# Kernel tuning notes

Measured on AMD Instinct MI355X. Metric: run time of the kernel, lower is better.

Reference implementation:

```python
import jax, jax.numpy as jnp
import numpy as np

B, S, D, H = 64, 512, 544, 1024  # batch, seq, state_dim+pb_dim, n_hid


def setup_inputs() -> dict:
    key = jax.random.key(0)
    k_x, k_wih, k_whh, k_bih, k_bhh = jax.random.split(key, 5)
    bound = 1.0 / np.sqrt(H)  # PyTorch LSTM uniform init range
    X = jax.random.normal(k_x, (B, S, D), dtype=jnp.float32)
    W_ih = jax.random.uniform(k_wih, (4 * H, D), jnp.float32, -bound, bound)
    W_hh = jax.random.uniform(k_whh, (4 * H, H), jnp.float32, -bound, bound)
    b_ih = jax.random.uniform(k_bih, (4 * H,), jnp.float32, -bound, bound)
    b_hh = jax.random.uniform(k_bhh, (4 * H,), jnp.float32, -bound, bound)
    return {"X": X, "W_ih": W_ih, "W_hh": W_hh, "b_ih": b_ih, "b_hh": b_hh}


def reference(X, W_ih, W_hh, b_ih, b_hh):
    # Faithful to PBRNN.forward: LSTM scanned over the sequence dim
    # (the torch code loops one timestep at a time; the math is a plain
    # single-layer LSTM from zero initial state). Returns final (h, c)
    # stacked as [2, B, H] — the only state forward() produces.
    n_batch = X.shape[0]
    n_hid = W_hh.shape[1]
    Xs = jnp.swapaxes(X, 0, 1)  # [S, B, D]
    # Precompute input projections for all timesteps: [S, B, 4H]
    x_proj = jnp.einsum('sbd,gd->sbg', Xs, W_ih) + (b_ih + b_hh)

    def step(carry, xp):
        h, c = carry
        gates = xp + h @ W_hh.T  # [B, 4H]
        i, f, g, o = jnp.split(gates, 4, axis=-1)  # PyTorch gate order i,f,g,o
        i = jax.nn.sigmoid(i)
        f = jax.nn.sigmoid(f)
        g = jnp.tanh(g)
        o = jax.nn.sigmoid(o)
        c = f * c + i * g
        h = o * jnp.tanh(c)
        return (h, c), None

    h0 = jnp.zeros((n_batch, n_hid), dtype=X.dtype)
    c0 = jnp.zeros((n_batch, n_hid), dtype=X.dtype)
    (h_n, c_n), _ = jax.lax.scan(step, (h0, c0), x_proj)
    return jnp.stack([h_n, c_n])  # [2, B, H]
```

## Files before the change

kernel.cpp:

```cpp
#include <hip/hip_runtime.h>
#include <hip/hip_bf16.h>


#define B_  64
#define S_  512
#define D_  544
#define H_  1024
#define CG_ 64
#define BG_ 4
#define GRID_ (CG_*BG_)

typedef __attribute__((ext_vector_type(8))) short bf16x8;
typedef __attribute__((ext_vector_type(4))) float f32x4;

__device__ inline ushort f2b(float x){
  unsigned u = __float_as_uint(x);
  u = (u + 0x7FFFu + ((u >> 16) & 1u)) >> 16;
  return (ushort)u;
}

__device__ inline bf16x8 pack8(float4 a, float4 b){
  bf16x8 r;
  r[0]=(short)f2b(a.x); r[1]=(short)f2b(a.y); r[2]=(short)f2b(a.z); r[3]=(short)f2b(a.w);
  r[4]=(short)f2b(b.x); r[5]=(short)f2b(b.y); r[6]=(short)f2b(b.z); r[7]=(short)f2b(b.w);
  return r;
}

__device__ inline unsigned long long ld64a(const unsigned long long* q){
  return __hip_atomic_load(q, __ATOMIC_RELAXED, __HIP_MEMORY_SCOPE_AGENT);
}

__device__ inline float sigm(float x){ return __builtin_amdgcn_rcpf(1.f + __expf(-x)); }
__device__ inline float tanh_(float x){ return 1.f - 2.f*__builtin_amdgcn_rcpf(1.f + __expf(2.f*x)); }

__global__ void cvt_x(const float* __restrict__ x, ushort* __restrict__ xb, int n4){
  int i = blockIdx.x*256 + threadIdx.x;
  if (i >= n4) return;
  float4 v = ((const float4*)x)[i];
  ushort4 o;
  o.x=f2b(v.x); o.y=f2b(v.y); o.z=f2b(v.z); o.w=f2b(v.w);
  ((ushort4*)xb)[i] = o;
}

__global__ __launch_bounds__(256,1) void lstm_persist(
    const float* __restrict__ Wih, const float* __restrict__ Whh,
    const float* __restrict__ bih, const float* __restrict__ bhh,
    const ushort* __restrict__ Xb,
    unsigned* thbuf,
    float* __restrict__ out)
{
  const int tid  = threadIdx.x;
  const int wave = tid >> 6;
  const int lane = tid & 63;
  const int c16  = lane & 15;
  const int quad = lane >> 4;
  const int cg   = blockIdx.x & (CG_-1);
  const int bg   = blockIdx.x >> 6;

  __shared__ float gates_s[4][64][17];

  bf16x8 whhf[4][8];
  #pragma unroll
  for (int mt = 0; mt < 4; ++mt){
    const size_t grow = (size_t)(mt*H_ + cg*16 + c16);
    #pragma unroll
    for (int i = 0; i < 8; ++i){
      int k = wave*256 + i*32 + quad*8;
      const float4* p = (const float4*)(Whh + grow*H_ + k);
      whhf[mt][i] = pack8(p[0], p[1]);
    }
  }
  bf16x8 wihf[4][5];
  #pragma unroll
  for (int mt = 0; mt < 4; ++mt){
    const size_t grow = (size_t)(mt*H_ + cg*16 + c16);
    #pragma unroll
    for (int ii = 0; ii < 5; ++ii){
      int it = wave + 4*ii;
      if (it < 17){
        int k = it*32 + quad*8;
        const float4* p = (const float4*)(Wih + grow*D_ + k);
        wihf[mt][ii] = pack8(p[0], p[1]);
      }
    }
  }

  const int uu = tid & 15;
  const int nn = tid >> 4;
  float bsum[4];
  #pragma unroll
  for (int g = 0; g < 4; ++g)
    bsum[g] = bih[g*H_ + cg*16 + uu] + bhh[g*H_ + cg*16 + uu];
  float cstate = 0.f;

  f32x4 acc[4];

  auto zacc = [&]{
    #pragma unroll
    for (int mt = 0; mt < 4; ++mt) acc[mt] = (f32x4){0.f,0.f,0.f,0.f};
  };
  auto xp_gemm = [&](int t){
    #pragma unroll
    for (int ii = 0; ii < 5; ++ii){
      int it = wave + 4*ii;
      if (it < 17){
        int k = it*32 + quad*8;
        bf16x8 b = *(const bf16x8*)(Xb + ((size_t)(bg*16 + c16)*S_ + t)*D_ + k);
        #pragma unroll
        for (int mt = 0; mt < 4; ++mt)
          acc[mt] = __builtin_amdgcn_mfma_f32_16x16x32_bf16(wihf[mt][ii], b, acc[mt], 0,0,0);
      }
    }
  };

  zacc();
  xp_gemm(0);

  const int obase = (bg*64 + wave*16 + (quad>>1))*256 + c16*16 + (quad&1)*8;

  for (int t = 0; t < S_; ++t){
    const unsigned* hp = thbuf + (t & 1) * (B_*H_);
    unsigned*       hn = thbuf + ((t & 1) ^ 1) * (B_*H_);

    {
      const unsigned tag = (unsigned)t & 0xffffu;
      const unsigned long long tmask = 0xffff0000ffff0000ull;
      const unsigned long long texp  = ((unsigned long long)tag << 16)
                                     | ((unsigned long long)tag << 48);
      unsigned long long q[8][4];
      #pragma unroll
      for (int i = 0; i < 8; ++i){
        const unsigned long long* p = (const unsigned long long*)(hp + obase + i*512);
        q[i][0] = ld64a(p);   q[i][1] = ld64a(p+1);
        q[i][2] = ld64a(p+2); q[i][3] = ld64a(p+3);
      }
      #pragma unroll
      for (int i = 0; i < 8; ++i){
        const unsigned long long* p = (const unsigned long long*)(hp + obase + i*512);
        long guard = 0;
        while ((((q[i][0]^texp)|(q[i][1]^texp)|(q[i][2]^texp)|(q[i][3]^texp)) & tmask) != 0ull){
          q[i][0] = ld64a(p);   q[i][1] = ld64a(p+1);
          q[i][2] = ld64a(p+2); q[i][3] = ld64a(p+3);
          if (++guard > (1L<<20)) break;
        }
        union { unsigned u[4]; bf16x8 v8; } eb;
        #pragma unroll
        for (int w = 0; w < 4; ++w){
          unsigned lo = (unsigned)q[i][w];
          unsigned hi = (unsigned)(q[i][w] >> 32);
          eb.u[w] = (lo & 0xffffu) | (hi << 16);
        }
        #pragma unroll
        for (int mt = 0; mt < 4; ++mt)
          acc[mt] = __builtin_amdgcn_mfma_f32_16x16x32_bf16(whhf[mt][i], eb.v8, acc[mt], 0,0,0);
      }
    }

    #pragma unroll
    for (int mt = 0; mt < 4; ++mt)
      #pragma unroll
      for (int r = 0; r < 4; ++r)
        gates_s[wave][mt*16 + quad*4 + r][c16] = acc[mt][r];
    __syncthreads();

    {
      float gsum[4];
      #pragma unroll
      for (int g = 0; g < 4; ++g){
        float s = bsum[g];
        #pragma unroll
        for (int q2 = 0; q2 < 4; ++q2) s += gates_s[q2][g*16 + uu][nn];
        gsum[g] = s;
      }
      float iv = sigm(gsum[0]), fv = sigm(gsum[1]), gv = tanh_(gsum[2]), ov = sigm(gsum[3]);
      float cn = fv*cstate + iv*gv;
      cstate = cn;
      float hv = ov*tanh_(cn);
      unsigned word = (((unsigned)(t+1) & 0xffffu) << 16) | (unsigned)f2b(hv);
      __hip_atomic_store(hn + (size_t)(bg*64 + cg)*256 + tid, word,
                         __ATOMIC_RELAXED, __HIP_MEMORY_SCOPE_AGENT);
      if (t == S_-1){
        out[(bg*16 + nn)*H_ + cg*16 + uu]          = hv;
        out[B_*H_ + (bg*16 + nn)*H_ + cg*16 + uu]  = cn;
      }
    }
    __syncthreads();

    if (t < S_-1){
      zacc();
      xp_gemm(t+1);
    }
  }
}

extern "C" void kernel_launch(void* const* d_in, const int* in_sizes, int n_in,
                              void* d_out, int out_size, void* d_ws, size_t ws_size,
                              hipStream_t stream) {
  const float* X   = (const float*)d_in[0];
  const float* Wih = (const float*)d_in[1];
  const float* Whh = (const float*)d_in[2];
  const float* bih = (const float*)d_in[3];
  const float* bhh = (const float*)d_in[4];
  float* out = (float*)d_out;

  char* ws = (char*)d_ws;
  const size_t THBUF_BYTES = 2ull * B_ * H_ * sizeof(unsigned);
  const size_t XB_OFF      = THBUF_BYTES;
  const size_t XB_BYTES    = (size_t)B_ * S_ * D_ * sizeof(ushort);
  if (ws_size < XB_OFF + XB_BYTES) return;

  unsigned* thbuf = (unsigned*)ws;
  ushort*   Xb    = (ushort*)(ws + XB_OFF);

  hipMemsetAsync(d_ws, 0, THBUF_BYTES, stream);

  int n4 = B_*S_*D_/4;
  cvt_x<<<(n4 + 255)/256, 256, 0, stream>>>(X, Xb, n4);
  lstm_persist<<<GRID_, 256, 0, stream>>>(Wih, Whh, bih, bhh, Xb, thbuf, out);
}
```

Before: 2.709 ms.

## Prefetch next-step X slice, double-buffer gate LDS, and poll h-chunks jointly

Measured after the change: 2.342 ms. 1.16x faster.

```diff
diff --git a/kernel.cpp b/kernel.cpp
--- a/kernel.cpp
+++ b/kernel.cpp
@@ -54,10 +54,10 @@
   const int lane = tid & 63;
   const int c16  = lane & 15;
   const int quad = lane >> 4;
-  const int cg   = blockIdx.x & (CG_-1);
-  const int bg   = blockIdx.x >> 6;
-
-  __shared__ float gates_s[4][64][17];
+  const int bg   = (blockIdx.x & 7) >> 1;
+  const int cg   = ((blockIdx.x >> 3) << 1) | (blockIdx.x & 1);
+
+  __shared__ float gates_s[2][4][64][17];
 
   bf16x8 whhf[4][8];
   #pragma unroll
@@ -94,27 +94,37 @@
   float cstate = 0.f;
 
   f32x4 acc[4];
+  bf16x8 xraw[5];
 
   auto zacc = [&]{
     #pragma unroll
     for (int mt = 0; mt < 4; ++mt) acc[mt] = (f32x4){0.f,0.f,0.f,0.f};
   };
-  auto xp_gemm = [&](int t){
+  auto ldx = [&](int t){
+    if (t >= S_) t = S_-1;
+    #pragma unroll
+    for (int ii = 0; ii < 5; ++ii){
+      int it = wave + 4*ii;
+      if (it < 17)
+        xraw[ii] = *(const bf16x8*)(Xb + ((size_t)(bg*16 + c16)*S_ + t)*D_ + it*32 + quad*8);
+    }
+  };
+  auto xp_mfma = [&]{
     #pragma unroll
     for (int ii = 0; ii < 5; ++ii){
       int it = wave + 4*ii;
       if (it < 17){
-        int k = it*32 + quad*8;
-        bf16x8 b = *(const bf16x8*)(Xb + ((size_t)(bg*16 + c16)*S_ + t)*D_ + k);
         #pragma unroll
         for (int mt = 0; mt < 4; ++mt)
-          acc[mt] = __builtin_amdgcn_mfma_f32_16x16x32_bf16(wihf[mt][ii], b, acc[mt], 0,0,0);
+          acc[mt] = __builtin_amdgcn_mfma_f32_16x16x32_bf16(wihf[mt][ii], xraw[ii], acc[mt], 0,0,0);
       }
     }
   };
 
+  ldx(0);
   zacc();
-  xp_gemm(0);
+  xp_mfma();
+  ldx(1);
 
   const int obase = (bg*64 + wave*16 + (quad>>1))*256 + c16*16 + (quad&1)*8;
 
@@ -122,45 +132,58 @@
     const unsigned* hp = thbuf + (t & 1) * (B_*H_);
     unsigned*       hn = thbuf + ((t & 1) ^ 1) * (B_*H_);
 
+    unsigned long long q[8][4];
     {
       const unsigned tag = (unsigned)t & 0xffffu;
       const unsigned long long tmask = 0xffff0000ffff0000ull;
       const unsigned long long texp  = ((unsigned long long)tag << 16)
                                      | ((unsigned long long)tag << 48);
-      unsigned long long q[8][4];
+      const unsigned long long* pb[8];
       #pragma unroll
       for (int i = 0; i < 8; ++i){
-        const unsigned long long* p = (const unsigned long long*)(hp + obase + i*512);
-        q[i][0] = ld64a(p);   q[i][1] = ld64a(p+1);
-        q[i][2] = ld64a(p+2); q[i][3] = ld64a(p+3);
-      }
-      #pragma unroll
-      for (int i = 0; i < 8; ++i){
-        const unsigned long long* p = (const unsigned long long*)(hp + obase + i*512);
-        long guard = 0;
-        while ((((q[i][0]^texp)|(q[i][1]^texp)|(q[i][2]^texp)|(q[i][3]^texp)) & tmask) != 0ull){
-          q[i][0] = ld64a(p);   q[i][1] = ld64a(p+1);
-          q[i][2] = ld64a(p+2); q[i][3] = ld64a(p+3);
-          if (++guard > (1L<<20)) break;
+        pb[i] = (const unsigned long long*)(hp + obase + i*512);
+        q[i][0] = ld64a(pb[i]);   q[i][1] = ld64a(pb[i]+1);
+        q[i][2] = ld64a(pb[i]+2); q[i][3] = ld64a(pb[i]+3);
+      }
+      unsigned stale = 0xffu;
+      long rounds = 0;
+      while (stale){
+        unsigned ns = 0;
+        #pragma unroll
+        for (int i = 0; i < 8; ++i){
+          if (stale & (1u << i)){
+            unsigned long long d = ((q[i][0]^texp)|(q[i][1]^texp)
+                                   |(q[i][2]^texp)|(q[i][3]^texp)) & tmask;
+            if (d != 0ull){
+              q[i][0] = ld64a(pb[i]);   q[i][1] = ld64a(pb[i]+1);
+              q[i][2] = ld64a(pb[i]+2); q[i][3] = ld64a(pb[i]+3);
+              ns |= (1u << i);
+            }
+          }
         }
-        union { unsigned u[4]; bf16x8 v8; } eb;
-        #pragma unroll
-        for (int w = 0; w < 4; ++w){
-          unsigned lo = (unsigned)q[i][w];
-          unsigned hi = (unsigned)(q[i][w] >> 32);
-          eb.u[w] = (lo & 0xffffu) | (hi << 16);
-        }
-        #pragma unroll
-        for (int mt = 0; mt < 4; ++mt)
-          acc[mt] = __builtin_amdgcn_mfma_f32_16x16x32_bf16(whhf[mt][i], eb.v8, acc[mt], 0,0,0);
-      }
+        stale = ns;
+        if (++rounds > (1L<<20)) break;
+      }
+    }
+    #pragma unroll
+    for (int i = 0; i < 8; ++i){
+      union { unsigned u[4]; bf16x8 v8; } eb;
+      #pragma unroll
+      for (int w = 0; w < 4; ++w){
+        unsigned lo = (unsigned)q[i][w];
+        unsigned hi = (unsigned)(q[i][w] >> 32);
+        eb.u[w] = (lo & 0xffffu) | (hi << 16);
+      }
+      #pragma unroll
+      for (int mt = 0; mt < 4; ++mt)
+        acc[mt] = __builtin_amdgcn_mfma_f32_16x16x32_bf16(whhf[mt][i], eb.v8, acc[mt], 0,0,0);
     }
 
     #pragma unroll
     for (int mt = 0; mt < 4; ++mt)
       #pragma unroll
       for (int r = 0; r < 4; ++r)
-        gates_s[wave][mt*16 + quad*4 + r][c16] = acc[mt][r];
+        gates_s[t & 1][wave][mt*16 + quad*4 + r][c16] = acc[mt][r];
     __syncthreads();
 
     {
@@ -169,7 +192,7 @@
       for (int g = 0; g < 4; ++g){
         float s = bsum[g];
         #pragma unroll
-        for (int q2 = 0; q2 < 4; ++q2) s += gates_s[q2][g*16 + uu][nn];
+        for (int q2 = 0; q2 < 4; ++q2) s += gates_s[t & 1][q2][g*16 + uu][nn];
         gsum[g] = s;
       }
       float iv = sigm(gsum[0]), fv = sigm(gsum[1]), gv = tanh_(gsum[2]), ov = sigm(gsum[3]);
@@ -184,11 +207,11 @@
         out[B_*H_ + (bg*16 + nn)*H_ + cg*16 + uu]  = cn;
       }
     }
-    __syncthreads();
 
     if (t < S_-1){
       zacc();
-      xp_gemm(t+1);
+      xp_mfma();
+      ldx(t + 2);
     }
   }
 }
```
